# Performance work log

Measured on AMD Instinct MI355X. Metric: run time of the kernel, lower is better.

Reference implementation:

```python
import jax, jax.numpy as jnp
import numpy as np

N, E = 4096, 16384
N_DIM, E_DIM, C_DIM = 128, 64, 128
IN_DIM = N_DIM + E_DIM + N_DIM  # 320


def leaky_relu(x):
    return jax.nn.leaky_relu(x, negative_slope=0.01)


def setup_inputs() -> dict:
    key = jax.random.key(0)
    ks = jax.random.split(key, 12)
    u_features = jax.random.normal(ks[0], (E, N_DIM), dtype=jnp.float32)
    v_features = jax.random.normal(ks[1], (E, N_DIM), dtype=jnp.float32)
    edge_features = jax.random.normal(ks[2], (E, E_DIM), dtype=jnp.float32)
    # incidence-like 0/1 matrix (node i <- edge j), ~4 edges per node on average
    node_edge_matrix = (jax.random.uniform(ks[3], (N, E)) < (4.0 / N)).astype(jnp.float32)
    node_edge_mask = jnp.where(node_edge_matrix > 0, 0.0, -1e9).astype(jnp.float32)
    s = 1.0 / np.sqrt(IN_DIM)
    W_e = jax.random.uniform(ks[4], (IN_DIM, E_DIM), minval=-s, maxval=s, dtype=jnp.float32)
    b_e = jax.random.uniform(ks[5], (E_DIM,), minval=-s, maxval=s, dtype=jnp.float32)
    W = jax.random.uniform(ks[6], (IN_DIM, C_DIM), minval=-s, maxval=s, dtype=jnp.float32)
    b = jax.random.uniform(ks[7], (C_DIM,), minval=-s, maxval=s, dtype=jnp.float32)
    sa = 1.0 / np.sqrt(E_DIM)
    W_a = jax.random.uniform(ks[8], (E_DIM, 1), minval=-sa, maxval=sa, dtype=jnp.float32)
    b_a = jax.random.uniform(ks[9], (1,), minval=-sa, maxval=sa, dtype=jnp.float32)
    return {
        "u_features": u_features, "v_features": v_features,
        "edge_features": edge_features,
        "node_edge_matrix": node_edge_matrix, "node_edge_mask": node_edge_mask,
        "W_e": W_e, "b_e": b_e, "W": W, "b": b, "W_a": W_a, "b_a": b_a,
    }


def reference(u_features, v_features, edge_features, node_edge_matrix,
              node_edge_mask, W_e, b_e, W, b, W_a, b_a):
    # edge update MLP: [E, 2n+e] -> [E, e]
    uev = jnp.concatenate([u_features, edge_features, v_features], axis=1)
    new_edge_features = leaky_relu(uev @ W_e + b_e)
    # neighbor message MLP: [E, 2n+e] -> [E, c]
    uev2 = jnp.concatenate([u_features, new_edge_features, v_features], axis=1)
    neighbor_features = leaky_relu(uev2 @ W + b)
    # per-edge attention scalar a: [E]
    a = leaky_relu(new_edge_features @ W_a + b_a).reshape(-1)
    # node_edge_matrix @ diag(a) is just a column-wise broadcast multiply
    node_edge_weight = node_edge_matrix * a[None, :] + node_edge_mask  # [N, E]
    node_edge_weight = jax.nn.softmax(node_edge_weight, axis=1)
    context_features = jax.nn.elu(node_edge_weight @ neighbor_features)  # [N, c]
    return (context_features, new_edge_features)
```

## Files before the change

### kernel.cpp

```cpp
#include <hip/hip_runtime.h>
#include <hip/hip_bf16.h>

#define N_NODES 4096
#define N_EDGES 16384
#define NDIM 128
#define EDIM 64
#define CDIM 128
#define INDIM 320
#define EDGES_PER_BLK 64
#define MLP_BLOCKS (N_EDGES / EDGES_PER_BLK)
#define LDA 328

typedef __attribute__((ext_vector_type(8))) short s8v;
typedef __attribute__((ext_vector_type(4))) float f4v;

__device__ __forceinline__ float leaky(float x) { return x > 0.f ? x : 0.01f * x; }

__device__ __forceinline__ short f2bf(float x) {
    unsigned u = __float_as_uint(x);
    unsigned r = (u + 0x7FFFu + ((u >> 16) & 1u)) >> 16;
    return (short)r;
}

__global__ __launch_bounds__(256) void prepack_kernel(
    const float* __restrict__ We, const float* __restrict__ W,
    short* __restrict__ Wep, short* __restrict__ Wp)
{
    int id = blockIdx.x * 256 + threadIdx.x;
    if (id < 2560) {
        int lane = id & 63, nt = (id >> 6) & 3, kt = id >> 8;
        int col = nt * 16 + (lane & 15);
        int krow = kt * 32 + (lane >> 4) * 8;
        s8v o;
        #pragma unroll
        for (int j = 0; j < 8; ++j) o[j] = f2bf(We[(krow + j) * 64 + col]);
        *(s8v*)&Wep[(size_t)id * 8] = o;
    } else if (id < 7680) {
        int id2 = id - 2560;
        int lane = id2 & 63, nt = (id2 >> 6) & 7, kt = id2 >> 9;
        int col = nt * 16 + (lane & 15);
        int krow = kt * 32 + (lane >> 4) * 8;
        s8v o;
        #pragma unroll
        for (int j = 0; j < 8; ++j) o[j] = f2bf(W[(krow + j) * 128 + col]);
        *(s8v*)&Wp[(size_t)id2 * 8] = o;
    }
}

__global__ __launch_bounds__(256) void edge_mlp_kernel(
    const float* __restrict__ u, const float* __restrict__ v,
    const float* __restrict__ ef,
    const short* __restrict__ Wep, const float* __restrict__ be,
    const short* __restrict__ Wp,  const float* __restrict__ b,
    const float* __restrict__ Wa,  const float* __restrict__ ba,
    float* __restrict__ out_ne,
    float* __restrict__ neighbor,
    float* __restrict__ a_out,
    float* __restrict__ colsum_partial)
{
    __shared__ short lds[EDGES_PER_BLK * LDA];
    __shared__ float red[4][128];
    const int tid  = threadIdx.x;
    const int e0   = blockIdx.x * EDGES_PER_BLK;
    const int w    = tid >> 6;
    const int lane = tid & 63;
    const int c16  = lane & 15;
    const int hi   = lane >> 4;

    {
        const float4* up = (const float4*)(u + (size_t)e0 * NDIM);
        #pragma unroll
        for (int i = 0; i < 8; ++i) {
            int f = i * 256 + tid;
            int row = f >> 5, k4 = f & 31;
            float4 val = up[f];
            short4 o = { f2bf(val.x), f2bf(val.y), f2bf(val.z), f2bf(val.w) };
            *(short4*)&lds[row * LDA + k4 * 4] = o;
        }
        const float4* vp = (const float4*)(v + (size_t)e0 * NDIM);
        #pragma unroll
        for (int i = 0; i < 8; ++i) {
            int f = i * 256 + tid;
            int row = f >> 5, k4 = f & 31;
            float4 val = vp[f];
            short4 o = { f2bf(val.x), f2bf(val.y), f2bf(val.z), f2bf(val.w) };
            *(short4*)&lds[row * LDA + 192 + k4 * 4] = o;
        }
        const float4* ep = (const float4*)(ef + (size_t)e0 * EDIM);
        #pragma unroll
        for (int i = 0; i < 4; ++i) {
            int f = i * 256 + tid;
            int row = f >> 4, k4 = f & 15;
            float4 val = ep[f];
            short4 o = { f2bf(val.x), f2bf(val.y), f2bf(val.z), f2bf(val.w) };
            *(short4*)&lds[row * LDA + 128 + k4 * 4] = o;
        }
    }
    __syncthreads();

    const short* arow = &lds[(16 * w + c16) * LDA];

    f4v acc1[4];
    #pragma unroll
    for (int nt = 0; nt < 4; ++nt) acc1[nt] = (f4v){0.f, 0.f, 0.f, 0.f};
    #pragma unroll
    for (int kt = 0; kt < 10; ++kt) {
        s8v af = *(const s8v*)(arow + kt * 32 + hi * 8);
        #pragma unroll
        for (int nt = 0; nt < 4; ++nt) {
            s8v bf = *(const s8v*)(Wep + ((size_t)(kt * 4 + nt) * 64 + lane) * 8);
            acc1[nt] = __builtin_amdgcn_mfma_f32_16x16x32_bf16(af, bf, acc1[nt], 0, 0, 0);
        }
    }

    float be_r[4], wa_r[4];
    #pragma unroll
    for (int nt = 0; nt < 4; ++nt) {
        be_r[nt] = be[nt * 16 + c16];
        wa_r[nt] = Wa[nt * 16 + c16];
    }
    float a_part[4] = {0.f, 0.f, 0.f, 0.f};
    #pragma unroll
    for (int nt = 0; nt < 4; ++nt) {
        #pragma unroll
        for (int r = 0; r < 4; ++r) {
            float nv = leaky(acc1[nt][r] + be_r[nt]);
            int lrow = 16 * w + hi * 4 + r;
            out_ne[(size_t)(e0 + lrow) * 64 + nt * 16 + c16] = nv;
            lds[lrow * LDA + 128 + nt * 16 + c16] = f2bf(nv);
            a_part[r] += nv * wa_r[nt];
        }
    }
    #pragma unroll
    for (int r = 0; r < 4; ++r) {
        #pragma unroll
        for (int off = 1; off < 16; off <<= 1)
            a_part[r] += __shfl_xor(a_part[r], off);
    }
    if (c16 == 0) {
        float ba0 = ba[0];
        #pragma unroll
        for (int r = 0; r < 4; ++r)
            a_out[e0 + 16 * w + hi * 4 + r] = leaky(a_part[r] + ba0);
    }

    f4v acc2[8];
    #pragma unroll
    for (int nt = 0; nt < 8; ++nt) acc2[nt] = (f4v){0.f, 0.f, 0.f, 0.f};
    #pragma unroll
    for (int kt = 0; kt < 10; ++kt) {
        s8v af = *(const s8v*)(arow + kt * 32 + hi * 8);
        #pragma unroll
        for (int nt = 0; nt < 8; ++nt) {
            s8v bf = *(const s8v*)(Wp + ((size_t)(kt * 8 + nt) * 64 + lane) * 8);
            acc2[nt] = __builtin_amdgcn_mfma_f32_16x16x32_bf16(af, bf, acc2[nt], 0, 0, 0);
        }
    }

    float b_r[8], cs[8];
    #pragma unroll
    for (int nt = 0; nt < 8; ++nt) { b_r[nt] = b[nt * 16 + c16]; cs[nt] = 0.f; }
    #pragma unroll
    for (int nt = 0; nt < 8; ++nt) {
        #pragma unroll
        for (int r = 0; r < 4; ++r) {
            float nv = leaky(acc2[nt][r] + b_r[nt]);
            int lrow = 16 * w + hi * 4 + r;
            neighbor[(size_t)(e0 + lrow) * 128 + nt * 16 + c16] = nv;
            cs[nt] += nv;
        }
    }
    #pragma unroll
    for (int nt = 0; nt < 8; ++nt) {
        cs[nt] += __shfl_xor(cs[nt], 16);
        cs[nt] += __shfl_xor(cs[nt], 32);
    }
    if (lane < 16) {
        #pragma unroll
        for (int nt = 0; nt < 8; ++nt) red[w][nt * 16 + lane] = cs[nt];
    }
    __syncthreads();
    if (tid < 128)
        colsum_partial[(size_t)blockIdx.x * 128 + tid] =
            red[0][tid] + red[1][tid] + red[2][tid] + red[3][tid];
}

__global__ __launch_bounds__(256) void scatter_softmax_kernel(
    const float* __restrict__ mat, const float* __restrict__ a,
    const float* __restrict__ neighbor,
    const float* __restrict__ colsum_partial,
    float* __restrict__ ctx)
{
    __shared__ int   js[1024];
    __shared__ float as[1024];
    __shared__ float ews[1024];
    __shared__ int   cnt;
    __shared__ float ctx_half[128];
    const int tid = threadIdx.x;
    const int row = blockIdx.x;
    if (tid == 0) cnt = 0;
    __syncthreads();

    const float4* rp = (const float4*)(mat + (size_t)row * N_EDGES);
    #pragma unroll 8
    for (int t = 0; t < 16; ++t) {
        int f = t * 256 + tid;
        float4 vv = rp[f];
        if (vv.x + vv.y + vv.z + vv.w != 0.f) {
            if (vv.x != 0.f) { int s = atomicAdd(&cnt, 1); if (s < 1024) js[s] = f * 4 + 0; }
            if (vv.y != 0.f) { int s = atomicAdd(&cnt, 1); if (s < 1024) js[s] = f * 4 + 1; }
            if (vv.z != 0.f) { int s = atomicAdd(&cnt, 1); if (s < 1024) js[s] = f * 4 + 2; }
            if (vv.w != 0.f) { int s = atomicAdd(&cnt, 1); if (s < 1024) js[s] = f * 4 + 3; }
        }
    }
    __syncthreads();
    int n = cnt; if (n > 1024) n = 1024;

    const int c    = tid & 127;
    const int half = tid >> 7;

    if (n > 0) {
        for (int t = tid; t < n; t += 256) as[t] = a[js[t]];
        __syncthreads();

        const int lane = tid & 63;
        float ls = 0.f;
        for (int t = lane; t < n; t += 64) {
            float e = __expf(as[t]);
            ews[t] = e;
            ls += e;
        }
        #pragma unroll
        for (int off = 32; off; off >>= 1) ls += __shfl_xor(ls, off);
        const float inv = 1.0f / ls;
        __syncthreads();

        float acc = 0.f;
        for (int t = half; t < n; t += 2)
            acc += ews[t] * neighbor[(size_t)js[t] * 128 + c];
        if (half == 0) ctx_half[c] = acc;
        __syncthreads();
        if (half == 1) {
            float tot = (ctx_half[c] + acc) * inv;
            ctx[(size_t)row * 128 + c] = tot > 0.f ? tot : expm1f(tot);
        }
    } else {
        float acc = 0.f;
        for (int p = half; p < MLP_BLOCKS; p += 2)
            acc += colsum_partial[(size_t)p * 128 + c];
        if (half == 0) ctx_half[c] = acc;
        __syncthreads();
        if (half == 1) {
            float tot = (ctx_half[c] + acc) * (1.0f / N_EDGES);
            ctx[(size_t)row * 128 + c] = tot > 0.f ? tot : expm1f(tot);
        }
    }
}

extern "C" void kernel_launch(void* const* d_in, const int* in_sizes, int n_in,
                              void* d_out, int out_size, void* d_ws, size_t ws_size,
                              hipStream_t stream) {
    const float* u   = (const float*)d_in[0];
    const float* v   = (const float*)d_in[1];
    const float* ef  = (const float*)d_in[2];
    const float* mat = (const float*)d_in[3];
    const float* We = (const float*)d_in[5];
    const float* be = (const float*)d_in[6];
    const float* W  = (const float*)d_in[7];
    const float* b  = (const float*)d_in[8];
    const float* Wa = (const float*)d_in[9];
    const float* ba = (const float*)d_in[10];

    float* out    = (float*)d_out;
    float* ctx    = out;
    float* out_ne = out + (size_t)N_NODES * CDIM;

    float* neighbor = (float*)d_ws;
    float* a_ws     = neighbor + (size_t)N_EDGES * CDIM;
    float* colsum_p = a_ws + N_EDGES;
    short* Wep      = (short*)(colsum_p + MLP_BLOCKS * 128);
    short* Wp       = Wep + 2560 * 8;

    prepack_kernel<<<30, 256, 0, stream>>>(We, W, Wep, Wp);
    edge_mlp_kernel<<<MLP_BLOCKS, 256, 0, stream>>>(
        u, v, ef, Wep, be, Wp, b, Wa, ba, out_ne, neighbor, a_ws, colsum_p);
    scatter_softmax_kernel<<<N_NODES, 256, 0, stream>>>(
        mat, a_ws, neighbor, colsum_p, ctx);
}
```

Baseline: 73.70 us.

## Overlap incidence-matrix scan with edge MLP and slim down gather kernel

Moves the scan of the 4096x16384 incidence matrix out of the softmax kernel and into extra blocks of the edge-MLP launch. The memory-bound scan can then run alongside the compute-bound MLP blocks, with nonzero indices and counts written to global workspace. The softmax/gather step becomes a 64-thread-per-row kernel that reads the compacted indices and processes two channels per lane with float2 loads. The cost is extra global traffic for the index lists and a heavier fused launch that mixes two block types.

Result: slower. 83.42 us (+13.2%).

```diff
diff --git a/kernel.cpp b/kernel.cpp
--- a/kernel.cpp
+++ b/kernel.cpp
@@ -10,6 +10,7 @@
 #define EDGES_PER_BLK 64
 #define MLP_BLOCKS (N_EDGES / EDGES_PER_BLK)
 #define LDA 328
+#define IDX_CAP 1024
 
 typedef __attribute__((ext_vector_type(8))) short s8v;
 typedef __attribute__((ext_vector_type(4))) float f4v;
@@ -47,20 +48,46 @@
     }
 }
 
-__global__ __launch_bounds__(256) void edge_mlp_kernel(
+__global__ __launch_bounds__(256) void fused_mlp_scan_kernel(
     const float* __restrict__ u, const float* __restrict__ v,
-    const float* __restrict__ ef,
+    const float* __restrict__ ef, const float* __restrict__ mat,
     const short* __restrict__ Wep, const float* __restrict__ be,
     const short* __restrict__ Wp,  const float* __restrict__ b,
     const float* __restrict__ Wa,  const float* __restrict__ ba,
     float* __restrict__ out_ne,
     float* __restrict__ neighbor,
     float* __restrict__ a_out,
-    float* __restrict__ colsum_partial)
+    float* __restrict__ colsum_partial,
+    int*   __restrict__ cnt_g,
+    int*   __restrict__ js_g)
 {
     __shared__ short lds[EDGES_PER_BLK * LDA];
     __shared__ float red[4][128];
-    const int tid  = threadIdx.x;
+    const int tid = threadIdx.x;
+
+    if (blockIdx.x >= MLP_BLOCKS) {
+        const int row = blockIdx.x - MLP_BLOCKS;
+        int* cnt = (int*)&lds[0];
+        if (tid == 0) *cnt = 0;
+        __syncthreads();
+        const float4* rp = (const float4*)(mat + (size_t)row * N_EDGES);
+        #pragma unroll 8
+        for (int t = 0; t < 16; ++t) {
+            int f = t * 256 + tid;
+            float4 vv = rp[f];
+            if (vv.x + vv.y + vv.z + vv.w != 0.f) {
+                int* base = js_g + (size_t)row * IDX_CAP;
+                if (vv.x != 0.f) { int s = atomicAdd(cnt, 1); if (s < IDX_CAP) base[s] = f * 4 + 0; }
+                if (vv.y != 0.f) { int s = atomicAdd(cnt, 1); if (s < IDX_CAP) base[s] = f * 4 + 1; }
+                if (vv.z != 0.f) { int s = atomicAdd(cnt, 1); if (s < IDX_CAP) base[s] = f * 4 + 2; }
+                if (vv.w != 0.f) { int s = atomicAdd(cnt, 1); if (s < IDX_CAP) base[s] = f * 4 + 3; }
+            }
+        }
+        __syncthreads();
+        if (tid == 0) cnt_g[row] = (*cnt < IDX_CAP) ? *cnt : IDX_CAP;
+        return;
+    }
+
     const int e0   = blockIdx.x * EDGES_PER_BLK;
     const int w    = tid >> 6;
     const int lane = tid & 63;
@@ -185,48 +212,26 @@
             red[0][tid] + red[1][tid] + red[2][tid] + red[3][tid];
 }
 
-__global__ __launch_bounds__(256) void scatter_softmax_kernel(
-    const float* __restrict__ mat, const float* __restrict__ a,
-    const float* __restrict__ neighbor,
+__global__ __launch_bounds__(64) void gather_kernel(
+    const int* __restrict__ cnt_g, const int* __restrict__ js_g,
+    const float* __restrict__ a, const float* __restrict__ neighbor,
     const float* __restrict__ colsum_partial,
     float* __restrict__ ctx)
 {
-    __shared__ int   js[1024];
-    __shared__ float as[1024];
-    __shared__ float ews[1024];
-    __shared__ int   cnt;
-    __shared__ float ctx_half[128];
-    const int tid = threadIdx.x;
-    const int row = blockIdx.x;
-    if (tid == 0) cnt = 0;
-    __syncthreads();
-
-    const float4* rp = (const float4*)(mat + (size_t)row * N_EDGES);
-    #pragma unroll 8
-    for (int t = 0; t < 16; ++t) {
-        int f = t * 256 + tid;
-        float4 vv = rp[f];
-        if (vv.x + vv.y + vv.z + vv.w != 0.f) {
-            if (vv.x != 0.f) { int s = atomicAdd(&cnt, 1); if (s < 1024) js[s] = f * 4 + 0; }
-            if (vv.y != 0.f) { int s = atomicAdd(&cnt, 1); if (s < 1024) js[s] = f * 4 + 1; }
-            if (vv.z != 0.f) { int s = atomicAdd(&cnt, 1); if (s < 1024) js[s] = f * 4 + 2; }
-            if (vv.w != 0.f) { int s = atomicAdd(&cnt, 1); if (s < 1024) js[s] = f * 4 + 3; }
-        }
-    }
-    __syncthreads();
-    int n = cnt; if (n > 1024) n = 1024;
-
-    const int c    = tid & 127;
-    const int half = tid >> 7;
+    __shared__ float ews[IDX_CAP];
+    __shared__ int   jsl[IDX_CAP];
+    const int row  = blockIdx.x;
+    const int lane = threadIdx.x;
+    const int n    = cnt_g[row];
+    const int c0   = lane * 2;
 
     if (n > 0) {
-        for (int t = tid; t < n; t += 256) as[t] = a[js[t]];
-        __syncthreads();
-
-        const int lane = tid & 63;
+        const int* base = js_g + (size_t)row * IDX_CAP;
         float ls = 0.f;
         for (int t = lane; t < n; t += 64) {
-            float e = __expf(as[t]);
+            int j = base[t];
+            jsl[t] = j;
+            float e = __expf(a[j]);
             ews[t] = e;
             ls += e;
         }
@@ -235,25 +240,25 @@
         const float inv = 1.0f / ls;
         __syncthreads();
 
-        float acc = 0.f;
-        for (int t = half; t < n; t += 2)
-            acc += ews[t] * neighbor[(size_t)js[t] * 128 + c];
-        if (half == 0) ctx_half[c] = acc;
-        __syncthreads();
-        if (half == 1) {
-            float tot = (ctx_half[c] + acc) * inv;
-            ctx[(size_t)row * 128 + c] = tot > 0.f ? tot : expm1f(tot);
-        }
+        float ax = 0.f, ay = 0.f;
+        for (int t = 0; t < n; ++t) {
+            float2 nv = *(const float2*)&neighbor[(size_t)jsl[t] * 128 + c0];
+            float e = ews[t];
+            ax += e * nv.x;
+            ay += e * nv.y;
+        }
+        ax *= inv; ay *= inv;
+        float2 o = { ax > 0.f ? ax : expm1f(ax), ay > 0.f ? ay : expm1f(ay) };
+        *(float2*)&ctx[(size_t)row * 128 + c0] = o;
     } else {
-        float acc = 0.f;
-        for (int p = half; p < MLP_BLOCKS; p += 2)
-            acc += colsum_partial[(size_t)p * 128 + c];
-        if (half == 0) ctx_half[c] = acc;
-        __syncthreads();
-        if (half == 1) {
-            float tot = (ctx_half[c] + acc) * (1.0f / N_EDGES);
-            ctx[(size_t)row * 128 + c] = tot > 0.f ? tot : expm1f(tot);
-        }
+        float ax = 0.f, ay = 0.f;
+        for (int p = 0; p < MLP_BLOCKS; ++p) {
+            ax += colsum_partial[(size_t)p * 128 + c0];
+            ay += colsum_partial[(size_t)p * 128 + c0 + 1];
+        }
+        ax *= (1.0f / N_EDGES); ay *= (1.0f / N_EDGES);
+        float2 o = { ax > 0.f ? ax : expm1f(ax), ay > 0.f ? ay : expm1f(ay) };
+        *(float2*)&ctx[(size_t)row * 128 + c0] = o;
     }
 }
 
@@ -280,10 +285,13 @@
     float* colsum_p = a_ws + N_EDGES;
     short* Wep      = (short*)(colsum_p + MLP_BLOCKS * 128);
     short* Wp       = Wep + 2560 * 8;
+    int*   cnt_g    = (int*)(Wp + 5120 * 8);
+    int*   js_g     = cnt_g + N_NODES;
 
     prepack_kernel<<<30, 256, 0, stream>>>(We, W, Wep, Wp);
-    edge_mlp_kernel<<<MLP_BLOCKS, 256, 0, stream>>>(
-        u, v, ef, Wep, be, Wp, b, Wa, ba, out_ne, neighbor, a_ws, colsum_p);
-    scatter_softmax_kernel<<<N_NODES, 256, 0, stream>>>(
-        mat, a_ws, neighbor, colsum_p, ctx);
-}
+    fused_mlp_scan_kernel<<<MLP_BLOCKS + N_NODES, 256, 0, stream>>>(
+        u, v, ef, mat, Wep, be, Wp, b, Wa, ba,
+        out_ne, neighbor, a_ws, colsum_p, cnt_g, js_g);
+    gather_kernel<<<N_NODES, 64, 0, stream>>>(
+        cnt_g, js_g, a_ws, neighbor, colsum_p, ctx);
+}
```
